# Kernel optimization log

Measured on AMD Instinct MI355X. Metric: run time of the kernel, lower is better.

Reference implementation:

```python
import jax, jax.numpy as jnp
import numpy as np

N_NODES = 100000
N_EDGES = 1600000
N_GRAPHS = 64


def setup_inputs() -> dict:
    key = jax.random.key(0)
    ks = jax.random.split(key, 6)
    x = jax.random.normal(ks[0], (N_NODES, 64), dtype=jnp.float32)
    edge_index = jax.random.randint(ks[1], (2, N_EDGES), 0, N_NODES, dtype=jnp.int64)
    batch = jnp.sort(jax.random.randint(ks[2], (N_NODES,), 0, N_GRAPHS, dtype=jnp.int64))
    W1 = jax.random.normal(ks[3], (64, 128), dtype=jnp.float32) * (1.0 / np.sqrt(64))
    b1 = jnp.zeros((128,), dtype=jnp.float32)
    ln_w = jnp.ones((128,), dtype=jnp.float32)
    ln_b = jnp.zeros((128,), dtype=jnp.float32)
    W2 = jax.random.normal(ks[4], (128, 64), dtype=jnp.float32) * (1.0 / np.sqrt(128))
    b2 = jnp.zeros((64,), dtype=jnp.float32)
    return {"x": x, "edge_index": edge_index, "batch": batch, "W1": W1, "b1": b1,
            "ln_w": ln_w, "ln_b": ln_b, "W2": W2, "b2": b2}


def _gcn_conv(h, row, col, n_nodes, W, b):
    # PyG GCNConv: linear transform, symmetric deg^-1/2 normalization, scatter-add at targets, bias.
    h = h @ W  # [N, out]
    ones = jnp.ones_like(col, dtype=h.dtype)
    deg = jax.ops.segment_sum(ones, col, num_segments=n_nodes)  # in-degree incl. self-loops
    dinv = jnp.where(deg > 0, jax.lax.rsqrt(deg), 0.0)
    norm = dinv[row] * dinv[col]  # [E']
    msg = h[row] * norm[:, None]  # gather + scale
    out = jax.ops.segment_sum(msg, col, num_segments=n_nodes)  # scatter-add
    return out + b


def _layer_norm(h, w, b, eps=1e-5):
    mu = jnp.mean(h, axis=-1, keepdims=True)
    var = jnp.mean(jnp.square(h - mu), axis=-1, keepdims=True)
    return (h - mu) * jax.lax.rsqrt(var + eps) * w + b


def reference(x, edge_index, batch, W1, b1, ln_w, ln_b, W2, b2):
    n = x.shape[0]
    # add self-loops (as each GCNConv does internally)
    loops = jnp.arange(n, dtype=edge_index.dtype)
    row = jnp.concatenate([edge_index[0], loops])
    col = jnp.concatenate([edge_index[1], loops])

    h = _gcn_conv(x, row, col, n, W1, b1)
    h = _layer_norm(h, ln_w, ln_b)
    h = jax.nn.relu(h)
    h = _gcn_conv(h, row, col, n, W2, b2)

    # global mean pool per graph
    sums = jax.ops.segment_sum(h, batch, num_segments=N_GRAPHS)
    counts = jax.ops.segment_sum(jnp.ones((n,), dtype=h.dtype), batch, num_segments=N_GRAPHS)
    g = sums / jnp.maximum(counts, 1.0)[:, None]
    return h, g
```

## Files before the change

### kernel.cpp

```cpp
#include <hip/hip_runtime.h>
#include <hip/hip_bf16.h>
#include <hip/hip_fp16.h>
#include <cstdint>

#define N_NODES 100000
#define N_EDGES 1600000
#define N_GRAPHS 64
#define F_IN 64
#define F_MID 128
#define F_OUT 64

typedef unsigned int uint32;

#define BK_SHIFT 10
#define BK_COLS (1 << BK_SHIFT)
#define NBUK ((N_NODES + BK_COLS - 1) >> BK_SHIFT)
#define BK_CAP 17408
#define EPB 4096
#define NPB ((N_EDGES + EPB - 1) / EPB)

__device__ __forceinline__ float ldF(const void* p, size_t i, int f32) {
    return f32 ? ((const float*)p)[i]
               : __bfloat162float(((const __hip_bfloat16*)p)[i]);
}
__device__ __forceinline__ int ldI(const void* p, size_t i, int i64) {
    return i64 ? (int)((const long long*)p)[i] : ((const int*)p)[i];
}
__device__ __forceinline__ void stF(void* p, size_t i, float v, int f32) {
    if (f32) ((float*)p)[i] = v;
    else     ((__hip_bfloat16*)p)[i] = __float2bfloat16(v);
}

union H2U { uint32 u; __half2 h; };
__device__ __forceinline__ float2 up16(uint32 u) {
    H2U c; c.u = u;
    return __half22float2(c.h);
}
__device__ __forceinline__ __half2 u2h(uint32 u) {
    H2U c; c.u = u;
    return c.h;
}
__device__ __forceinline__ uint32 pk16(float a, float b) {
    H2U c; c.h = __floats2half2_rn(a, b);
    return c.u;
}
__device__ __forceinline__ unsigned short bfbits(float f) {
    __hip_bfloat16 b = __float2bfloat16(f);
    return *(unsigned short*)&b;
}

struct Acc8 { float2 p0, p1, p2, p3; };

__device__ __forceinline__ void accum(Acc8& A, const uint4 d) {
    const float2 f0 = up16(d.x), f1 = up16(d.y), f2 = up16(d.z), f3 = up16(d.w);
    A.p0.x += f0.x; A.p0.y += f0.y;
    A.p1.x += f1.x; A.p1.y += f1.y;
    A.p2.x += f2.x; A.p2.y += f2.y;
    A.p3.x += f3.x; A.p3.y += f3.y;
}

__device__ __forceinline__ void oct_gather(const int* __restrict__ sp,
                                           const uint32* __restrict__ rows,
                                           const int beg, const int end,
                                           const int q, const int obase,
                                           Acc8& A) {
    int pre = sp[beg + q];
    int myidx = (beg + q < end) ? pre : N_NODES;
    for (int jj = beg; jj < end; jj += 8) {
        const int cur = myidx;
        const int nx = jj + 8 + q;
        pre = sp[nx];
        myidx = (nx < end) ? pre : N_NODES;
        const int i0 = __shfl(cur, obase | 0, 64);
        const int i1 = __shfl(cur, obase | 1, 64);
        const int i2 = __shfl(cur, obase | 2, 64);
        const int i3 = __shfl(cur, obase | 3, 64);
        const int i4 = __shfl(cur, obase | 4, 64);
        const int i5 = __shfl(cur, obase | 5, 64);
        const int i6 = __shfl(cur, obase | 6, 64);
        const int i7 = __shfl(cur, obase | 7, 64);
        const uint32 qo = (uint32)(q << 2);
        const uint4 d0 = *(const uint4*)(rows + ((uint32)i0 * 32u + qo));
        const uint4 d1 = *(const uint4*)(rows + ((uint32)i1 * 32u + qo));
        const uint4 d2 = *(const uint4*)(rows + ((uint32)i2 * 32u + qo));
        const uint4 d3 = *(const uint4*)(rows + ((uint32)i3 * 32u + qo));
        const uint4 d4 = *(const uint4*)(rows + ((uint32)i4 * 32u + qo));
        const uint4 d5 = *(const uint4*)(rows + ((uint32)i5 * 32u + qo));
        const uint4 d6 = *(const uint4*)(rows + ((uint32)i6 * 32u + qo));
        const uint4 d7 = *(const uint4*)(rows + ((uint32)i7 * 32u + qo));
        accum(A, d0); accum(A, d1); accum(A, d2); accum(A, d3);
        accum(A, d4); accum(A, d5); accum(A, d6); accum(A, d7);
    }
}

__global__ void GCNEncoder_77214922048129_kernel(const void* x, const void* ei,
                                                 int* flags, int* gcur) {
    __shared__ int cnt_weird, cnt_zero;
    if (threadIdx.x == 0) { cnt_weird = 0; cnt_zero = 0; }
    if (threadIdx.x < NBUK) gcur[threadIdx.x] = threadIdx.x * BK_CAP;
    __syncthreads();
    const unsigned short* u = (const unsigned short*)x;
    int w = 0;
    for (int i = threadIdx.x; i < 2048; i += 256) {
        int e = (u[i] >> 7) & 0xFF;
        if (e == 0xFF || e >= 159 || (e > 0 && e <= 95)) w++;
    }
    atomicAdd(&cnt_weird, w);
    const int* ii = (const int*)ei;
    int z = 0;
    for (int i = threadIdx.x; i < 128; i += 256) {
        if (ii[2 * i + 1] == 0) z++;
    }
    atomicAdd(&cnt_zero, z);
    __syncthreads();
    if (threadIdx.x == 0) {
        flags[0] = (cnt_weird > 64) ? 1 : 0;
        flags[1] = (cnt_zero > 64) ? 1 : 0;
    }
}

__global__ __launch_bounds__(256) void k_part(const void* __restrict__ ei,
                                              uint2* __restrict__ part,
                                              int* __restrict__ gcur,
                                              const int* __restrict__ flags) {
    const int i64 = flags[1];
    __shared__ uint2 est[EPB];
    __shared__ int cnt[NBUK], base_[NBUK], cur[NBUK];
    const int t = threadIdx.x;
    const int e0 = blockIdx.x * EPB;
    const int ne = min(EPB, N_EDGES - e0);
    for (int i = t; i < NBUK; i += 256) { cnt[i] = 0; cur[i] = 0; }
    __syncthreads();
    for (int i = t; i < ne; i += 256) {
        const int e = e0 + i;
        const int r = ldI(ei, e, i64);
        const int c = ldI(ei, (size_t)N_EDGES + e, i64);
        est[i] = make_uint2((uint32)r, (uint32)c);
        atomicAdd(&cnt[c >> BK_SHIFT], 1);
    }
    __syncthreads();
    for (int b = t; b < NBUK; b += 256)
        base_[b] = (cnt[b] > 0) ? atomicAdd(&gcur[b], cnt[b]) : 0;
    __syncthreads();
    for (int i = t; i < ne; i += 256) {
        const uint2 rc = est[i];
        const int b = (int)(rc.y >> BK_SHIFT);
        const int off = atomicAdd(&cur[b], 1);
        const int pos = base_[b] + off;
        if (pos < (b + 1) * BK_CAP) part[pos] = rc;
    }
}

__global__ __launch_bounds__(256) void k_bdeg(const uint2* __restrict__ part,
                                              const int* __restrict__ gcur,
                                              int* __restrict__ deg) {
    __shared__ int h[BK_COLS];
    const int b = blockIdx.x;
    const int t = threadIdx.x;
    for (int i = t; i < BK_COLS; i += 256) h[i] = 0;
    __syncthreads();
    const int beg = b * BK_CAP;
    const int cnt = min(gcur[b] - beg, BK_CAP);
    for (int i = t; i < cnt; i += 256)
        atomicAdd(&h[part[beg + i].y & (BK_COLS - 1)], 1);
    __syncthreads();
    const int cbase = b << BK_SHIFT;
    for (int i = t; i < BK_COLS; i += 256)
        if (cbase + i < N_NODES) deg[cbase + i] = h[i];
}

__global__ __launch_bounds__(256) void k_fill(const uint2* __restrict__ part,
                                              const int* __restrict__ gcur,
                                              const int* __restrict__ rowptr,
                                              int* __restrict__ src) {
    __shared__ int cur[BK_COLS];
    const int b = blockIdx.x;
    const int t = threadIdx.x;
    const int cbase = b << BK_SHIFT;
    for (int i = t; i < BK_COLS; i += 256)
        cur[i] = (cbase + i < N_NODES) ? rowptr[cbase + i] : 0;
    __syncthreads();
    const int beg = b * BK_CAP;
    const int cnt = min(gcur[b] - beg, BK_CAP);
    for (int i = t; i < cnt; i += 256) {
        const uint2 rc = part[beg + i];
        const int pos = atomicAdd(&cur[rc.y & (BK_COLS - 1)], 1);
        src[pos] = (int)rc.x;
    }
}

#define NB_SCAN ((N_NODES + 255) / 256)

__global__ __launch_bounds__(256) void k_bsum(const int* __restrict__ deg,
                                              int* __restrict__ bsum,
                                              float* __restrict__ dinv) {
    __shared__ int sh[256];
    int idx = blockIdx.x * 256 + threadIdx.x;
    int d = 0;
    if (idx < N_NODES) {
        d = deg[idx];
        dinv[idx] = rsqrtf((float)d + 1.0f);
    }
    sh[threadIdx.x] = d;
    __syncthreads();
#pragma unroll
    for (int off = 128; off > 0; off >>= 1) {
        if (threadIdx.x < off) sh[threadIdx.x] += sh[threadIdx.x + off];
        __syncthreads();
    }
    if (threadIdx.x == 0) bsum[blockIdx.x] = sh[0];
}

__global__ __launch_bounds__(512) void k_bscan(const int* __restrict__ bsum,
                                               int* __restrict__ bbase) {
    __shared__ int sh[512];
    const int t = threadIdx.x;
    sh[t] = (t < NB_SCAN) ? bsum[t] : 0;
    __syncthreads();
    for (int off = 1; off < 512; off <<= 1) {
        int v = (t >= off) ? sh[t - off] : 0;
        __syncthreads();
        sh[t] += v;
        __syncthreads();
    }
    if (t < NB_SCAN) bbase[t] = (t == 0) ? 0 : sh[t - 1];
}

__global__ __launch_bounds__(256) void k_rowptr(const int* __restrict__ deg,
                                                const int* __restrict__ bbase,
                                                int* __restrict__ rowptr) {
    __shared__ int sh[256];
    const int t = threadIdx.x;
    const int idx = blockIdx.x * 256 + t;
    const int d = (idx < N_NODES) ? deg[idx] : 0;
    sh[t] = d;
    __syncthreads();
    for (int off = 1; off < 256; off <<= 1) {
        int v = (t >= off) ? sh[t - off] : 0;
        __syncthreads();
        sh[t] += v;
        __syncthreads();
    }
    if (idx < N_NODES) rowptr[idx] = bbase[blockIdx.x] + sh[t] - d;
    if (idx == 0) rowptr[N_NODES] = N_EDGES;
}

__global__ __launch_bounds__(256) void k_scale(const void* __restrict__ x,
                                               const float* __restrict__ dinv,
                                               uint32* __restrict__ xs16,
                                               uint32* __restrict__ a2u,
                                               const int* __restrict__ flags) {
    const int F32 = flags[0];
    int idx = blockIdx.x * blockDim.x + threadIdx.x;
    if (idx < N_NODES * 32) {
        int n = idx >> 5;
        float dv = dinv[n];
        float a = ldF(x, (size_t)idx * 2, F32) * dv;
        float b = ldF(x, (size_t)idx * 2 + 1, F32) * dv;
        xs16[idx] = pk16(a, b);
    } else if (idx < (N_NODES + 1) * 32) {
        xs16[idx] = 0u;
        a2u[idx] = 0u;
    }
}

#define G1W 8
__global__ __launch_bounds__(64 * G1W) void k_gather1(
    const int* __restrict__ rowptr, const int* __restrict__ src,
    const uint32* __restrict__ xsu, const float* __restrict__ dinv,
    const void* __restrict__ b1, const void* __restrict__ lnw,
    const void* __restrict__ lnb, const void* __restrict__ W1,
    const void* __restrict__ W2, uint32* __restrict__ a2u,
    const int* __restrict__ flags) {
    const int F32 = flags[0];
    __shared__ uint2  w1d[32 * 64];
    __shared__ uint2  w2q[32 * 64];
    __shared__ float b1s[F_MID], lnws[F_MID], lnbs[F_MID];
    __shared__ uint32 aggp[G1W][8][32];
    __shared__ uint32 usp[G1W][64];
    for (int i = threadIdx.x; i < 32 * 64; i += 64 * G1W) {
        const int k2 = i >> 6, f = i & 63;
        uint2 w;
        w.x = pk16(ldF(W1, (size_t)(2 * k2) * F_MID + f, F32),
                   ldF(W1, (size_t)(2 * k2 + 1) * F_MID + f, F32));
        w.y = pk16(ldF(W1, (size_t)(2 * k2) * F_MID + f + 64, F32),
                   ldF(W1, (size_t)(2 * k2 + 1) * F_MID + f + 64, F32));
        w1d[i] = w;
    }
    for (int i = threadIdx.x; i < 32 * 64; i += 64 * G1W) {
        const int k4 = i >> 6, f = i & 63;
        uint2 w;
        w.x = pk16(ldF(W2, (size_t)(4 * k4) * F_OUT + f, F32),
                   ldF(W2, (size_t)(4 * k4 + 1) * F_OUT + f, F32));
        w.y = pk16(ldF(W2, (size_t)(4 * k4 + 2) * F_OUT + f, F32),
                   ldF(W2, (size_t)(4 * k4 + 3) * F_OUT + f, F32));
        w2q[i] = w;
    }
    if (threadIdx.x < F_MID) {
        b1s[threadIdx.x] = ldF(b1, threadIdx.x, F32);
        lnws[threadIdx.x] = ldF(lnw, threadIdx.x, F32);
        lnbs[threadIdx.x] = ldF(lnb, threadIdx.x, F32);
    }
    __syncthreads();
    const int wid = threadIdx.x >> 6;
    const int lane = threadIdx.x & 63;
    const int q = lane & 7;
    const int oct = lane >> 3;
    const int obase = lane & 56;
    const int gw = (blockIdx.x * (64 * G1W) + threadIdx.x) >> 6;
    const int totw = (gridDim.x * (64 * G1W)) >> 6;
    const __half2 hz = __float2half2_rn(0.f);
    for (int nb = gw * 8; nb < N_NODES; nb += totw * 8) {
        const int n = nb + oct;
        const int nc = (n < N_NODES) ? n : (N_NODES - 1);
        int beg = rowptr[nc], end = rowptr[nc + 1];
        if (n >= N_NODES) { beg = 0; end = 0; }
        const uint32 nself = (n < N_NODES) ? (uint32)n : (uint32)N_NODES;
        const uint4 sd = *(const uint4*)(xsu + (nself * 32u + (uint32)(q << 2)));
        Acc8 A = {{0.f, 0.f}, {0.f, 0.f}, {0.f, 0.f}, {0.f, 0.f}};
        oct_gather(src, xsu, beg, end, q, obase, A);
        accum(A, sd);
        uint4 pkd;
        pkd.x = pk16(A.p0.x, A.p0.y);
        pkd.y = pk16(A.p1.x, A.p1.y);
        pkd.z = pk16(A.p2.x, A.p2.y);
        pkd.w = pk16(A.p3.x, A.p3.y);
        *(uint4*)&aggp[wid][oct][q * 4] = pkd;
        for (int c = 0; c < 8; ++c) {
            const int node = nb + c;
            if (node >= N_NODES) break;
            const float dv = dinv[node];
            __half2 hc0 = hz, hc1 = hz;
            float g0 = 0.f, g1 = 0.f;
#pragma unroll
            for (int qq = 0; qq < 8; ++qq) {
                const uint4 aq = ((const uint4*)aggp[wid][c])[qq];
#pragma unroll
                for (int j = 0; j < 4; ++j) {
                    const uint32 av = (j == 0) ? aq.x : (j == 1) ? aq.y : (j == 2) ? aq.z : aq.w;
                    const uint2 wv = w1d[(qq * 4 + j) * 64 + lane];
                    hc0 = __hfma2(u2h(av), u2h(wv.x), hc0);
                    hc1 = __hfma2(u2h(av), u2h(wv.y), hc1);
                }
                if (qq & 1) {
                    float2 p;
                    p = __half22float2(hc0); g0 += p.x + p.y; hc0 = hz;
                    p = __half22float2(hc1); g1 += p.x + p.y; hc1 = hz;
                }
            }
            const float t0 = g0 * dv + b1s[lane];
            const float t1 = g1 * dv + b1s[lane + 64];
            float s = t0 + t1;
#pragma unroll
            for (int off = 32; off > 0; off >>= 1) s += __shfl_xor(s, off, 64);
            const float mu = s * (1.f / 128.f);
            const float d0 = t0 - mu, d1 = t1 - mu;
            float v = d0 * d0 + d1 * d1;
#pragma unroll
            for (int off = 32; off > 0; off >>= 1) v += __shfl_xor(v, off, 64);
            const float rstd = rsqrtf(v * (1.f / 128.f) + 1e-5f);
            const float u0 = fmaxf(d0 * rstd * lnws[lane] + lnbs[lane], 0.f);
            const float u1 = fmaxf(d1 * rstd * lnws[lane + 64] + lnbs[lane + 64], 0.f);
            const int praw = (int)pk16(u0, u1);
            const int ia = __shfl(praw, (2 * lane) & 63, 64);
            const int ib = __shfl(praw, (2 * lane + 1) & 63, 64);
            const float2 fa = up16((uint32)ia), fb = up16((uint32)ib);
            const float ux = (lane < 32) ? fa.x : fa.y;
            const float uy = (lane < 32) ? fb.x : fb.y;
            usp[wid][lane] = pk16(ux, uy);
            __half2 hc = hz;
            float facc = 0.f;
#pragma unroll
            for (int qq = 0; qq < 16; ++qq) {
                const uint4 uq = ((const uint4*)usp[wid])[qq];
                const uint2 wv0 = w2q[(2 * qq) * 64 + lane];
                const uint2 wv1 = w2q[(2 * qq + 1) * 64 + lane];
                hc = __hfma2(u2h(uq.x), u2h(wv0.x), hc);
                hc = __hfma2(u2h(uq.y), u2h(wv0.y), hc);
                hc = __hfma2(u2h(uq.z), u2h(wv1.x), hc);
                hc = __hfma2(u2h(uq.w), u2h(wv1.y), hc);
                if ((qq & 3) == 3) {
                    const float2 p = __half22float2(hc);
                    facc += p.x + p.y;
                    hc = hz;
                }
            }
            const float a2 = facc * dv;
            const float e  = __shfl(a2, (2 * lane) & 63, 64);
            const float f2 = __shfl(a2, (2 * lane + 1) & 63, 64);
            if (lane < 32) a2u[(size_t)node * 32 + lane] = pk16(e, f2);
        }
    }
}

__global__ __launch_bounds__(256) void k_gather2(
    const int* __restrict__ rowptr, const int* __restrict__ src,
    const uint32* __restrict__ a2u, const float* __restrict__ dinv,
    const void* __restrict__ b2, void* __restrict__ out,
    const int* __restrict__ flags) {
    const int F32 = flags[0];
    const int lane = threadIdx.x & 63;
    const int q = lane & 7;
    const int oct = lane >> 3;
    const int obase = lane & 56;
    const float bb0 = ldF(b2, q * 8 + 0, F32), bb1 = ldF(b2, q * 8 + 1, F32);
    const float bb2 = ldF(b2, q * 8 + 2, F32), bb3 = ldF(b2, q * 8 + 3, F32);
    const float bb4 = ldF(b2, q * 8 + 4, F32), bb5 = ldF(b2, q * 8 + 5, F32);
    const float bb6 = ldF(b2, q * 8 + 6, F32), bb7 = ldF(b2, q * 8 + 7, F32);
    const int gw = (blockIdx.x * 256 + threadIdx.x) >> 6;
    const int totw = (gridDim.x * 256) >> 6;
    for (int nb = gw * 8; nb < N_NODES; nb += totw * 8) {
        const int n = nb + oct;
        const int nc = (n < N_NODES) ? n : (N_NODES - 1);
        int beg = rowptr[nc], end = rowptr[nc + 1];
        if (n >= N_NODES) { beg = 0; end = 0; }
        const uint32 nself = (n < N_NODES) ? (uint32)n : (uint32)N_NODES;
        const uint4 sd = *(const uint4*)(a2u + (nself * 32u + (uint32)(q << 2)));
        const float dv = dinv[nc];
        Acc8 A = {{0.f, 0.f}, {0.f, 0.f}, {0.f, 0.f}, {0.f, 0.f}};
        oct_gather(src, a2u, beg, end, q, obase, A);
        accum(A, sd);
        const float r0 = A.p0.x * dv + bb0, r1 = A.p0.y * dv + bb1;
        const float r2 = A.p1.x * dv + bb2, r3 = A.p1.y * dv + bb3;
        const float r4 = A.p2.x * dv + bb4, r5 = A.p2.y * dv + bb5;
        const float r6 = A.p3.x * dv + bb6, r7 = A.p3.y * dv + bb7;
        if (n < N_NODES) {
            if (F32) {
                float4 o0; o0.x = r0; o0.y = r1; o0.z = r2; o0.w = r3;
                float4 o1; o1.x = r4; o1.y = r5; o1.z = r6; o1.w = r7;
                ((float4*)out)[(size_t)n * 16 + (q << 1)]     = o0;
                ((float4*)out)[(size_t)n * 16 + (q << 1) + 1] = o1;
            } else {
                uint4 ub;
                ub.x = ((uint32)bfbits(r1) << 16) | (uint32)bfbits(r0);
                ub.y = ((uint32)bfbits(r3) << 16) | (uint32)bfbits(r2);
                ub.z = ((uint32)bfbits(r5) << 16) | (uint32)bfbits(r4);
                ub.w = ((uint32)bfbits(r7) << 16) | (uint32)bfbits(r6);
                ((uint4*)out)[(size_t)n * 8 + q] = ub;
            }
        }
    }
}

__global__ __launch_bounds__(256) void k_pool(const void* __restrict__ hout,
                                              const void* __restrict__ batch,
                                              float* __restrict__ gsum,
                                              const int* __restrict__ flags) {
    const int F32 = flags[0];
    const int i64 = flags[1];
    const int wid = (blockIdx.x * blockDim.x + threadIdx.x) >> 6;
    const int lane = threadIdx.x & 63;
    const int nwaves = (gridDim.x * blockDim.x) >> 6;
    const int per = (N_NODES + nwaves - 1) / nwaves;
    const int start = wid * per;
    const int end = min(start + per, N_NODES);
    if (start >= end) return;
    float acc = 0.f;
    int gcur = ldI(batch, start, i64);
    for (int n = start; n < end; ++n) {
        int g = ldI(batch, n, i64);
        if (g != gcur) {
            atomicAdd(&gsum[gcur * 64 + lane], acc);
            acc = 0.f;
            gcur = g;
        }
        acc += ldF(hout, (size_t)n * 64 + lane, F32);
    }
    atomicAdd(&gsum[gcur * 64 + lane], acc);
}

__global__ void k_gout(const float* __restrict__ gsum, const void* __restrict__ batch,
                       void* __restrict__ out, const int* __restrict__ flags) {
    const int F32 = flags[0];
    const int i64 = flags[1];
    int idx = blockIdx.x * blockDim.x + threadIdx.x;
    if (idx < N_GRAPHS * 64) {
        int g = idx >> 6;
        int lo = 0, hi = N_NODES;
        while (lo < hi) { int m = (lo + hi) >> 1; if (ldI(batch, m, i64) < g) lo = m + 1; else hi = m; }
        int lb = lo;
        lo = 0; hi = N_NODES;
        while (lo < hi) { int m = (lo + hi) >> 1; if (ldI(batch, m, i64) <= g) lo = m + 1; else hi = m; }
        float c = (float)max(lo - lb, 1);
        stF(out, (size_t)N_NODES * F_OUT + idx, gsum[idx] / c, F32);
    }
}

extern "C" void kernel_launch(void* const* d_in, const int* in_sizes, int n_in,
                              void* d_out, int out_size, void* d_ws, size_t ws_size,
                              hipStream_t stream) {
    const void* x   = d_in[0];
    const void* ei  = d_in[1];
    const void* bat = d_in[2];
    const void* W1  = d_in[3];
    const void* b1  = d_in[4];
    const void* lnw = d_in[5];
    const void* lnb = d_in[6];
    const void* W2  = d_in[7];
    const void* b2  = d_in[8];

    char* ws = (char*)d_ws;
    size_t o = 0;
    auto alloc = [&](size_t bytes) { size_t r = o; o += (bytes + 255) & ~(size_t)255; return r; };
    int*    flags  = (int*)   (ws + alloc(2 * 4));
    float*  dinv   = (float*) (ws + alloc((size_t)N_NODES * 4));
    int*    deg    = (int*)   (ws + alloc((size_t)N_NODES * 4));
    int*    rowptr = (int*)   (ws + alloc((size_t)(N_NODES + 1) * 4));
    int*    bsum   = (int*)   (ws + alloc((size_t)NB_SCAN * 4));
    int*    bbase  = (int*)   (ws + alloc((size_t)NB_SCAN * 4));
    int*    srcidx = (int*)   (ws + alloc((size_t)(N_EDGES + 64) * 4));
    uint32* xs16   = (uint32*)(ws + alloc((size_t)(N_NODES + 1) * 32 * 4));
    uint32* a2u    = (uint32*)(ws + alloc((size_t)(N_NODES + 1) * 32 * 4));
    float*  gsum   = (float*) (ws + alloc((size_t)N_GRAPHS * 64 * 4));
    uint2*  part   = (uint2*) (ws + alloc((size_t)NBUK * BK_CAP * 8));
    int*    gcur   = (int*)   (ws + alloc((size_t)NBUK * 4));

    hipMemsetAsync(gsum, 0, (size_t)N_GRAPHS * 64 * 4, stream);

    GCNEncoder_77214922048129_kernel<<<1, 256, 0, stream>>>(x, ei, flags, gcur);
    k_part<<<NPB, 256, 0, stream>>>(ei, part, gcur, flags);
    k_bdeg<<<NBUK, 256, 0, stream>>>(part, gcur, deg);
    k_bsum<<<NB_SCAN, 256, 0, stream>>>(deg, bsum, dinv);
    k_bscan<<<1, 512, 0, stream>>>(bsum, bbase);
    k_rowptr<<<NB_SCAN, 256, 0, stream>>>(deg, bbase, rowptr);
    k_fill<<<NBUK, 256, 0, stream>>>(part, gcur, rowptr, srcidx);
    k_scale<<<((N_NODES + 1) * 32 + 255) / 256, 256, 0, stream>>>(x, dinv, xs16, a2u, flags);
    k_gather1<<<1563, 64 * G1W, 0, stream>>>(rowptr, srcidx, xs16, dinv, b1, lnw, lnb,
                                             W1, W2, a2u, flags);
    k_gather2<<<3125, 256, 0, stream>>>(rowptr, srcidx, a2u, dinv, b2, d_out, flags);
    k_pool<<<512, 256, 0, stream>>>(d_out, bat, gsum, flags);
    k_gout<<<(N_GRAPHS * 64 + 255) / 256, 256, 0, stream>>>(gsum, bat, d_out, flags);
}
```

Measured before the change: 364.8 us.

## Sub-sort CSR neighbors into source-range segments for gather locality

The bucket histogram and fill kernels now split each destination's neighbor list into 8 segments by source-node range and store per-segment counts packed as bytes. The gather kernels then walk the segments in order, so that across a wavefront the 8 concurrent nodes tend to touch source rows in similar address ranges, which should improve cache locality. Bucket width is halved to fit the larger shared-memory histogram. This costs per-segment batch padding in the gathers, since partial batches now occur per segment rather than per node, and it assumes each per-segment count fits in 8 bits.

```diff
diff --git a/kernel.cpp b/kernel.cpp
--- a/kernel.cpp
+++ b/kernel.cpp
@@ -9,13 +9,14 @@
 #define F_IN 64
 #define F_MID 128
 #define F_OUT 64
+#define NSEG 8
 
 typedef unsigned int uint32;
 
-#define BK_SHIFT 10
+#define BK_SHIFT 9
 #define BK_COLS (1 << BK_SHIFT)
 #define NBUK ((N_NODES + BK_COLS - 1) >> BK_SHIFT)
-#define BK_CAP 17408
+#define BK_CAP 9216
 #define EPB 4096
 #define NPB ((N_EDGES + EPB - 1) / EPB)
 
@@ -29,6 +30,10 @@
 __device__ __forceinline__ void stF(void* p, size_t i, float v, int f32) {
     if (f32) ((float*)p)[i] = v;
     else     ((__hip_bfloat16*)p)[i] = __float2bfloat16(v);
+}
+
+__device__ __forceinline__ int segof(uint32 r) {
+    return (int)((r * (uint32)NSEG) / (uint32)N_NODES);
 }
 
 union H2U { uint32 u; __half2 h; };
@@ -59,37 +64,49 @@
     A.p3.x += f3.x; A.p3.y += f3.y;
 }
 
-__device__ __forceinline__ void oct_gather(const int* __restrict__ sp,
-                                           const uint32* __restrict__ rows,
-                                           const int beg, const int end,
-                                           const int q, const int obase,
-                                           Acc8& A) {
-    int pre = sp[beg + q];
-    int myidx = (beg + q < end) ? pre : N_NODES;
-    for (int jj = beg; jj < end; jj += 8) {
-        const int cur = myidx;
-        const int nx = jj + 8 + q;
-        pre = sp[nx];
-        myidx = (nx < end) ? pre : N_NODES;
-        const int i0 = __shfl(cur, obase | 0, 64);
-        const int i1 = __shfl(cur, obase | 1, 64);
-        const int i2 = __shfl(cur, obase | 2, 64);
-        const int i3 = __shfl(cur, obase | 3, 64);
-        const int i4 = __shfl(cur, obase | 4, 64);
-        const int i5 = __shfl(cur, obase | 5, 64);
-        const int i6 = __shfl(cur, obase | 6, 64);
-        const int i7 = __shfl(cur, obase | 7, 64);
-        const uint32 qo = (uint32)(q << 2);
-        const uint4 d0 = *(const uint4*)(rows + ((uint32)i0 * 32u + qo));
-        const uint4 d1 = *(const uint4*)(rows + ((uint32)i1 * 32u + qo));
-        const uint4 d2 = *(const uint4*)(rows + ((uint32)i2 * 32u + qo));
-        const uint4 d3 = *(const uint4*)(rows + ((uint32)i3 * 32u + qo));
-        const uint4 d4 = *(const uint4*)(rows + ((uint32)i4 * 32u + qo));
-        const uint4 d5 = *(const uint4*)(rows + ((uint32)i5 * 32u + qo));
-        const uint4 d6 = *(const uint4*)(rows + ((uint32)i6 * 32u + qo));
-        const uint4 d7 = *(const uint4*)(rows + ((uint32)i7 * 32u + qo));
-        accum(A, d0); accum(A, d1); accum(A, d2); accum(A, d3);
-        accum(A, d4); accum(A, d5); accum(A, d6); accum(A, d7);
+__device__ __forceinline__ void oct_batch(const uint32* __restrict__ rows,
+                                          const int cur, const int obase,
+                                          const uint32 qo, Acc8& A) {
+    const int i0 = __shfl(cur, obase | 0, 64);
+    const int i1 = __shfl(cur, obase | 1, 64);
+    const int i2 = __shfl(cur, obase | 2, 64);
+    const int i3 = __shfl(cur, obase | 3, 64);
+    const int i4 = __shfl(cur, obase | 4, 64);
+    const int i5 = __shfl(cur, obase | 5, 64);
+    const int i6 = __shfl(cur, obase | 6, 64);
+    const int i7 = __shfl(cur, obase | 7, 64);
+    const uint4 d0 = *(const uint4*)(rows + ((uint32)i0 * 32u + qo));
+    const uint4 d1 = *(const uint4*)(rows + ((uint32)i1 * 32u + qo));
+    const uint4 d2 = *(const uint4*)(rows + ((uint32)i2 * 32u + qo));
+    const uint4 d3 = *(const uint4*)(rows + ((uint32)i3 * 32u + qo));
+    const uint4 d4 = *(const uint4*)(rows + ((uint32)i4 * 32u + qo));
+    const uint4 d5 = *(const uint4*)(rows + ((uint32)i5 * 32u + qo));
+    const uint4 d6 = *(const uint4*)(rows + ((uint32)i6 * 32u + qo));
+    const uint4 d7 = *(const uint4*)(rows + ((uint32)i7 * 32u + qo));
+    accum(A, d0); accum(A, d1); accum(A, d2); accum(A, d3);
+    accum(A, d4); accum(A, d5); accum(A, d6); accum(A, d7);
+}
+
+__device__ __forceinline__ void oct_gather_seg(const int* __restrict__ sp,
+                                               const uint32* __restrict__ rows,
+                                               int curb, const uint2 sc,
+                                               const int q, const int obase,
+                                               Acc8& A) {
+    const uint32 qo = (uint32)(q << 2);
+    int t = sp[curb + q];
+#pragma unroll
+    for (int s = 0; s < NSEG; ++s) {
+        const uint32 w = (s < 4) ? sc.x : sc.y;
+        const int cnt = (int)((w >> ((s & 3) * 8)) & 0xFFu);
+        for (int o = 0; o < cnt; o += 8) {
+            const int rem = cnt - o;
+            const int nxt = (rem > 8) ? (curb + o + 8) : (curb + cnt);
+            const int tn = sp[nxt + q];
+            const int cur = (q < rem) ? t : N_NODES;
+            oct_batch(rows, cur, obase, qo, A);
+            t = tn;
+        }
+        curb += cnt;
     }
 }
 
@@ -153,38 +170,66 @@
 
 __global__ __launch_bounds__(256) void k_bdeg(const uint2* __restrict__ part,
                                               const int* __restrict__ gcur,
-                                              int* __restrict__ deg) {
-    __shared__ int h[BK_COLS];
+                                              int* __restrict__ deg,
+                                              uint2* __restrict__ seg8) {
+    __shared__ uint32 hs[BK_COLS * NSEG];
     const int b = blockIdx.x;
     const int t = threadIdx.x;
-    for (int i = t; i < BK_COLS; i += 256) h[i] = 0;
-    __syncthreads();
-    const int beg = b * BK_CAP;
-    const int cnt = min(gcur[b] - beg, BK_CAP);
-    for (int i = t; i < cnt; i += 256)
-        atomicAdd(&h[part[beg + i].y & (BK_COLS - 1)], 1);
-    __syncthreads();
-    const int cbase = b << BK_SHIFT;
-    for (int i = t; i < BK_COLS; i += 256)
-        if (cbase + i < N_NODES) deg[cbase + i] = h[i];
-}
-
-__global__ __launch_bounds__(256) void k_fill(const uint2* __restrict__ part,
-                                              const int* __restrict__ gcur,
-                                              const int* __restrict__ rowptr,
-                                              int* __restrict__ src) {
-    __shared__ int cur[BK_COLS];
-    const int b = blockIdx.x;
-    const int t = threadIdx.x;
-    const int cbase = b << BK_SHIFT;
-    for (int i = t; i < BK_COLS; i += 256)
-        cur[i] = (cbase + i < N_NODES) ? rowptr[cbase + i] : 0;
+    for (int i = t; i < BK_COLS * NSEG; i += 256) hs[i] = 0u;
     __syncthreads();
     const int beg = b * BK_CAP;
     const int cnt = min(gcur[b] - beg, BK_CAP);
     for (int i = t; i < cnt; i += 256) {
         const uint2 rc = part[beg + i];
-        const int pos = atomicAdd(&cur[rc.y & (BK_COLS - 1)], 1);
+        atomicAdd(&hs[(int)(rc.y & (BK_COLS - 1)) * NSEG + segof(rc.x)], 1u);
+    }
+    __syncthreads();
+    const int cbase = b << BK_SHIFT;
+    for (int c = t; c < BK_COLS; c += 256) {
+        const int col = cbase + c;
+        if (col < N_NODES) {
+            const uint32 h0 = hs[c * 8 + 0], h1 = hs[c * 8 + 1];
+            const uint32 h2 = hs[c * 8 + 2], h3 = hs[c * 8 + 3];
+            const uint32 h4 = hs[c * 8 + 4], h5 = hs[c * 8 + 5];
+            const uint32 h6 = hs[c * 8 + 6], h7 = hs[c * 8 + 7];
+            deg[col] = (int)(h0 + h1 + h2 + h3 + h4 + h5 + h6 + h7);
+            uint2 pk;
+            pk.x = h0 | (h1 << 8) | (h2 << 16) | (h3 << 24);
+            pk.y = h4 | (h5 << 8) | (h6 << 16) | (h7 << 24);
+            seg8[col] = pk;
+        }
+    }
+}
+
+__global__ __launch_bounds__(256) void k_fill(const uint2* __restrict__ part,
+                                              const int* __restrict__ gcur,
+                                              const int* __restrict__ rowptr,
+                                              const uint2* __restrict__ seg8,
+                                              int* __restrict__ src) {
+    __shared__ int cur[BK_COLS * NSEG];
+    const int b = blockIdx.x;
+    const int t = threadIdx.x;
+    const int cbase = b << BK_SHIFT;
+    for (int c = t; c < BK_COLS; c += 256) {
+        const int col = cbase + c;
+        int base = 0;
+        uint2 sc = make_uint2(0u, 0u);
+        if (col < N_NODES) { base = rowptr[col]; sc = seg8[col]; }
+        cur[c * 8 + 0] = base; base += (int)(sc.x & 0xFF);
+        cur[c * 8 + 1] = base; base += (int)((sc.x >> 8) & 0xFF);
+        cur[c * 8 + 2] = base; base += (int)((sc.x >> 16) & 0xFF);
+        cur[c * 8 + 3] = base; base += (int)((sc.x >> 24) & 0xFF);
+        cur[c * 8 + 4] = base; base += (int)(sc.y & 0xFF);
+        cur[c * 8 + 5] = base; base += (int)((sc.y >> 8) & 0xFF);
+        cur[c * 8 + 6] = base; base += (int)((sc.y >> 16) & 0xFF);
+        cur[c * 8 + 7] = base;
+    }
+    __syncthreads();
+    const int beg = b * BK_CAP;
+    const int cnt = min(gcur[b] - beg, BK_CAP);
+    for (int i = t; i < cnt; i += 256) {
+        const uint2 rc = part[beg + i];
+        const int pos = atomicAdd(&cur[(int)(rc.y & (BK_COLS - 1)) * NSEG + segof(rc.x)], 1);
         src[pos] = (int)rc.x;
     }
 }
@@ -267,6 +312,7 @@
 #define G1W 8
 __global__ __launch_bounds__(64 * G1W) void k_gather1(
     const int* __restrict__ rowptr, const int* __restrict__ src,
+    const uint2* __restrict__ seg8,
     const uint32* __restrict__ xsu, const float* __restrict__ dinv,
     const void* __restrict__ b1, const void* __restrict__ lnw,
     const void* __restrict__ lnb, const void* __restrict__ W1,
@@ -313,12 +359,13 @@
     for (int nb = gw * 8; nb < N_NODES; nb += totw * 8) {
         const int n = nb + oct;
         const int nc = (n < N_NODES) ? n : (N_NODES - 1);
-        int beg = rowptr[nc], end = rowptr[nc + 1];
-        if (n >= N_NODES) { beg = 0; end = 0; }
+        const int curb = rowptr[nc];
+        uint2 sc = make_uint2(0u, 0u);
+        if (n < N_NODES) sc = seg8[n];
         const uint32 nself = (n < N_NODES) ? (uint32)n : (uint32)N_NODES;
         const uint4 sd = *(const uint4*)(xsu + (nself * 32u + (uint32)(q << 2)));
         Acc8 A = {{0.f, 0.f}, {0.f, 0.f}, {0.f, 0.f}, {0.f, 0.f}};
-        oct_gather(src, xsu, beg, end, q, obase, A);
+        oct_gather_seg(src, xsu, curb, sc, q, obase, A);
         accum(A, sd);
         uint4 pkd;
         pkd.x = pk16(A.p0.x, A.p0.y);
@@ -395,6 +442,7 @@
 
 __global__ __launch_bounds__(256) void k_gather2(
     const int* __restrict__ rowptr, const int* __restrict__ src,
+    const uint2* __restrict__ seg8,
     const uint32* __restrict__ a2u, const float* __restrict__ dinv,
     const void* __restrict__ b2, void* __restrict__ out,
     const int* __restrict__ flags) {
@@ -412,13 +460,14 @@
     for (int nb = gw * 8; nb < N_NODES; nb += totw * 8) {
         const int n = nb + oct;
         const int nc = (n < N_NODES) ? n : (N_NODES - 1);
-        int beg = rowptr[nc], end = rowptr[nc + 1];
-        if (n >= N_NODES) { beg = 0; end = 0; }
+        const int curb = rowptr[nc];
+        uint2 sc = make_uint2(0u, 0u);
+        if (n < N_NODES) sc = seg8[n];
         const uint32 nself = (n < N_NODES) ? (uint32)n : (uint32)N_NODES;
         const uint4 sd = *(const uint4*)(a2u + (nself * 32u + (uint32)(q << 2)));
         const float dv = dinv[nc];
         Acc8 A = {{0.f, 0.f}, {0.f, 0.f}, {0.f, 0.f}, {0.f, 0.f}};
-        oct_gather(src, a2u, beg, end, q, obase, A);
+        oct_gather_seg(src, a2u, curb, sc, q, obase, A);
         accum(A, sd);
         const float r0 = A.p0.x * dv + bb0, r1 = A.p0.y * dv + bb1;
         const float r2 = A.p1.x * dv + bb2, r3 = A.p1.y * dv + bb3;
@@ -509,6 +558,7 @@
     int*    bsum   = (int*)   (ws + alloc((size_t)NB_SCAN * 4));
     int*    bbase  = (int*)   (ws + alloc((size_t)NB_SCAN * 4));
     int*    srcidx = (int*)   (ws + alloc((size_t)(N_EDGES + 64) * 4));
+    uint2*  seg8   = (uint2*) (ws + alloc((size_t)N_NODES * 8));
     uint32* xs16   = (uint32*)(ws + alloc((size_t)(N_NODES + 1) * 32 * 4));
     uint32* a2u    = (uint32*)(ws + alloc((size_t)(N_NODES + 1) * 32 * 4));
     float*  gsum   = (float*) (ws + alloc((size_t)N_GRAPHS * 64 * 4));
@@ -519,15 +569,15 @@
 
     GCNEncoder_77214922048129_kernel<<<1, 256, 0, stream>>>(x, ei, flags, gcur);
     k_part<<<NPB, 256, 0, stream>>>(ei, part, gcur, flags);
-    k_bdeg<<<NBUK, 256, 0, stream>>>(part, gcur, deg);
+    k_bdeg<<<NBUK, 256, 0, stream>>>(part, gcur, deg, seg8);
     k_bsum<<<NB_SCAN, 256, 0, stream>>>(deg, bsum, dinv);
     k_bscan<<<1, 512, 0, stream>>>(bsum, bbase);
     k_rowptr<<<NB_SCAN, 256, 0, stream>>>(deg, bbase, rowptr);
-    k_fill<<<NBUK, 256, 0, stream>>>(part, gcur, rowptr, srcidx);
+    k_fill<<<NBUK, 256, 0, stream>>>(part, gcur, rowptr, seg8, srcidx);
     k_scale<<<((N_NODES + 1) * 32 + 255) / 256, 256, 0, stream>>>(x, dinv, xs16, a2u, flags);
-    k_gather1<<<1563, 64 * G1W, 0, stream>>>(rowptr, srcidx, xs16, dinv, b1, lnw, lnb,
-                                             W1, W2, a2u, flags);
-    k_gather2<<<3125, 256, 0, stream>>>(rowptr, srcidx, a2u, dinv, b2, d_out, flags);
+    k_gather1<<<1563, 64 * G1W, 0, stream>>>(rowptr, srcidx, seg8, xs16, dinv, b1, lnw,
+                                             lnb, W1, W2, a2u, flags);
+    k_gather2<<<3125, 256, 0, stream>>>(rowptr, srcidx, seg8, a2u, dinv, b2, d_out, flags);
     k_pool<<<512, 256, 0, stream>>>(d_out, bat, gsum, flags);
     k_gout<<<(N_GRAPHS * 64 + 255) / 256, 256, 0, stream>>>(gsum, bat, d_out, flags);
 }
```

After: 361.6 us. Within noise of the previous version (-0.9%).
